# Kernel tuning notes

Hardware: AMD Instinct MI355X
Metric: run time of the kernel (lower is better)

Reference implementation:

```python
import jax, jax.numpy as jnp
import numpy as np

N = 50000
E = 1600000
D_IN, D_EMB, D_H, D_OUT, HEADS = 128, 128, 128, 64, 2


def setup_inputs() -> dict:
    key = jax.random.key(0)
    ks = jax.random.split(key, 12)
    return {
        "x": jax.random.normal(ks[0], (N, D_IN), jnp.float32),
        "edge_index": jax.random.randint(ks[1], (2, E), 0, N, dtype=jnp.int32),
        "node_indices": jnp.arange(N, dtype=jnp.int32),
        "emb": jax.random.normal(ks[2], (N, D_EMB), jnp.float32) * 0.1,
        "W_gcn": jax.random.normal(ks[3], (D_IN + D_EMB, D_H), jnp.float32) * 0.06,
        "b_gcn": jnp.zeros((D_H,), jnp.float32),
        "W_sage_l": jax.random.normal(ks[4], (D_H, D_H), jnp.float32) * 0.08,
        "W_sage_r": jax.random.normal(ks[5], (D_H, D_H), jnp.float32) * 0.08,
        "b_sage": jnp.zeros((D_H,), jnp.float32),
        "W_gat": jax.random.normal(ks[6], (D_H, HEADS, D_H), jnp.float32) * 0.08,
        "att_src": jax.random.normal(ks[7], (HEADS, D_H), jnp.float32) * 0.1,
        "att_dst": jax.random.normal(ks[8], (HEADS, D_H), jnp.float32) * 0.1,
        "b_gat": jnp.zeros((D_H,), jnp.float32),
        "W_out": jax.random.normal(ks[9], (D_H, D_OUT), jnp.float32) * 0.08,
        "b_out": jnp.zeros((D_OUT,), jnp.float32),
    }


def _forward(x, edge_index, node_indices, emb, W_gcn, b_gcn,
             W_sage_l, W_sage_r, b_sage, W_gat, att_src, att_dst, b_gat,
             W_out, b_out):
    n = x.shape[0]
    seg = jax.ops.segment_sum
    loops = jnp.arange(n, dtype=edge_index.dtype)

    # node2vec embedding lookup + concat
    h = jnp.concatenate([x, emb[node_indices]], axis=1)  # [N, D_IN+D_EMB]

    # --- GCNConv (symmetric norm, self loops) ---
    src = jnp.concatenate([edge_index[0], loops])
    dst = jnp.concatenate([edge_index[1], loops])
    deg = seg(jnp.ones_like(dst, jnp.float32), dst, num_segments=n)
    dinv = jnp.where(deg > 0, jax.lax.rsqrt(jnp.maximum(deg, 1.0)), 0.0)
    norm = dinv[src] * dinv[dst]                     # [E+N]
    hW = h @ W_gcn                                   # [N, D_H]
    h = seg(hW[src] * norm[:, None], dst, num_segments=n) + b_gcn
    h = jax.nn.relu(h)

    # --- SAGEConv (mean aggregation, no self loops) ---
    s, d = edge_index[0], edge_index[1]
    agg = seg(h[s], d, num_segments=n)
    cnt = seg(jnp.ones_like(d, jnp.float32), d, num_segments=n)
    mean = agg / jnp.maximum(cnt, 1.0)[:, None]
    h = mean @ W_sage_l + h @ W_sage_r + b_sage
    h = jax.nn.relu(h)

    # --- GATConv heads=2, concat=False (mean over heads), self loops ---
    xW = jnp.einsum('nd,dhc->nhc', h, W_gat)         # [N, H, D_H]
    a_src = jnp.einsum('nhc,hc->nh', xW, att_src)    # [N, H]
    a_dst = jnp.einsum('nhc,hc->nh', xW, att_dst)
    alpha = jax.nn.leaky_relu(a_src[src] + a_dst[dst], 0.2)  # [E+N, H]
    amax = jax.ops.segment_max(alpha, dst, num_segments=n)
    alpha = jnp.exp(alpha - amax[dst])
    asum = seg(alpha, dst, num_segments=n)
    alpha = alpha / (asum[dst] + 1e-16)
    out = seg(xW[src] * alpha[:, :, None], dst, num_segments=n)  # [N, H, D_H]
    h = jax.nn.relu(out.mean(axis=1) + b_gat)

    return h @ W_out + b_out


def reference(x, edge_index, node_indices, emb, W_gcn, b_gcn,
              W_sage_l, W_sage_r, b_sage, W_gat, att_src, att_dst, b_gat,
              W_out, b_out):
    return _forward(x, edge_index, node_indices, emb, W_gcn, b_gcn,
                    W_sage_l, W_sage_r, b_sage, W_gat, att_src, att_dst, b_gat,
                    W_out, b_out)
```

## Files before the change

### kernel.cpp

```cpp
#include <hip/hip_runtime.h>


typedef short bf16x8 __attribute__((ext_vector_type(8)));
typedef float f32x4  __attribute__((ext_vector_type(4)));

static __device__ __forceinline__ float leaky02(float x) {
    return x > 0.f ? x : 0.2f * x;
}
static __device__ __forceinline__ unsigned short f2bf(float f) {
    unsigned u = __float_as_uint(f);
    u = (u + 0x7FFFu + ((u >> 16) & 1u)) >> 16;
    return (unsigned short)u;
}
static __device__ __forceinline__ float bf2f(unsigned short h) {
    return __uint_as_float(((unsigned)h) << 16);
}
static __device__ __forceinline__ float4 bf4(ushort4 h) {
    return make_float4(bf2f(h.x), bf2f(h.y), bf2f(h.z), bf2f(h.w));
}
static __device__ __forceinline__ void split_bf(float v, unsigned short& h,
                                                unsigned short& l) {
    unsigned u = __float_as_uint(v);
    unsigned uh = u & 0xFFFF0000u;
    h = (unsigned short)(uh >> 16);
    l = f2bf(v - __uint_as_float(uh));
}

__global__ void deg_edges(const int* __restrict__ dst, int* __restrict__ degi, int E) {
    int e = blockIdx.x * blockDim.x + threadIdx.x;
    if (e < E) atomicAdd(&degi[dst[e]], 1);
}

__global__ __launch_bounds__(256)
void scan_part_norm(const int* __restrict__ degi, int* __restrict__ partial,
                    float* __restrict__ dinv, float* __restrict__ icnt, int n)
{
    int t = threadIdx.x;
    int base = blockIdx.x * 1024 + t * 4;
    int s = 0;
#pragma unroll
    for (int i = 0; i < 4; ++i) {
        int g = base + i;
        if (g < n) {
            int de = degi[g];
            s += de;
            dinv[g] = rsqrtf((float)(de + 1));
            icnt[g] = 1.0f / (float)(de > 1 ? de : 1);
        }
    }
#pragma unroll
    for (int m = 32; m > 0; m >>= 1) s += __shfl_xor(s, m, 64);
    __shared__ int wsum[4];
    if ((t & 63) == 0) wsum[t >> 6] = s;
    __syncthreads();
    if (t == 0) partial[blockIdx.x] = wsum[0] + wsum[1] + wsum[2] + wsum[3];
}

__global__ __launch_bounds__(64)
void scan_offsets(int* __restrict__ partial, int nb)
{
    int t = threadIdx.x;
    int carry = 0;
    for (int base = 0; base < nb; base += 64) {
        int i = base + t;
        int v = (i < nb) ? partial[i] : 0;
        int incl = v;
#pragma unroll
        for (int m = 1; m < 64; m <<= 1) {
            int o = __shfl_up(incl, m, 64);
            if (t >= m) incl += o;
        }
        if (i < nb) partial[i] = incl - v + carry;
        carry += __shfl(incl, 63, 64);
    }
}

__global__ __launch_bounds__(256)
void scan_write(const int* __restrict__ degi, const int* __restrict__ partial,
                int* __restrict__ rowptr, int n)
{
    __shared__ int tmp[256];
    int t = threadIdx.x;
    int base = blockIdx.x * 1024 + t * 4;
    int v[4]; int s = 0;
#pragma unroll
    for (int i = 0; i < 4; ++i) {
        int g = base + i;
        v[i] = (g < n) ? degi[g] : 0;
        s += v[i];
    }
    tmp[t] = s;
    __syncthreads();
    for (int off = 1; off < 256; off <<= 1) {
        int a = (t >= off) ? tmp[t - off] : 0;
        __syncthreads();
        tmp[t] += a;
        __syncthreads();
    }
    int run = tmp[t] - s + partial[blockIdx.x];
#pragma unroll
    for (int i = 0; i < 4; ++i) {
        int g = base + i;
        if (g < n) rowptr[g] = run;
        run += v[i];
    }
}

__global__ void csr_fill(const int* __restrict__ src, const int* __restrict__ dst,
                         int* __restrict__ rowptr, int* __restrict__ csr, int E)
{
    int e = blockIdx.x * blockDim.x + threadIdx.x;
    if (e >= E) return;
    int d = dst[e];
    int pos = atomicAdd(&rowptr[d], 1);
    csr[pos] = src[e];
}

template<bool HAS_A2, bool RELU, bool HAS_BIAS, bool HAS_IDX, bool SCALE,
         bool ATT, bool OUT_BF16, bool A_BF16>
__global__ __launch_bounds__(256)
void gemm_mfma(const void* __restrict__ A1, const float* __restrict__ W1,
               const void* __restrict__ A2, const float* __restrict__ W2,
               const int* __restrict__ idx2, const float* __restrict__ bias,
               const float* __restrict__ scale,
               const float* __restrict__ att_src, const float* __restrict__ att_dst,
               float* __restrict__ a_s, float* __restrict__ a_d,
               float* __restrict__ C, int nrows, int ncW, int ncC)
{
    __shared__ unsigned short ABh[8][65][8];
    __shared__ unsigned short WBh[8][65][8], WBl[8][65][8];
    const int t    = threadIdx.x;
    const int lane = t & 63;
    const int wv   = t >> 6;
    const int l15  = lane & 15;
    const int lg   = lane >> 4;
    const int row0 = blockIdx.x * 128;
    const int colOff = blockIdx.y * 128;

    f32x4 acc[2][8];
#pragma unroll
    for (int mt = 0; mt < 2; ++mt)
#pragma unroll
        for (int nt = 0; nt < 8; ++nt) acc[mt][nt] = (f32x4){0.f, 0.f, 0.f, 0.f};

    const int npass = HAS_A2 ? 2 : 1;
    for (int p = 0; p < npass; ++p) {
        const void* A = (p == 0) ? A1 : A2;
        const float* W = (p == 0) ? W1 : W2;
        for (int kt = 0; kt < 4; ++kt) {
            if (A_BF16) {
                const unsigned short* Ab = (const unsigned short*)A;
#pragma unroll
                for (int i = 0; i < 2; ++i) {
                    int f = i * 256 + t;
                    int r = f >> 2, kq = f & 3;
                    int row = row0 + r; if (row >= nrows) row = nrows - 1;
                    int arow = (p == 1 && HAS_IDX) ? idx2[row] : row;
                    bf16x8 v = *(const bf16x8*)(Ab + (size_t)arow * 128 + kt * 32 + kq * 8);
                    *(bf16x8*)&ABh[r >> 4][(r & 15) + (kq << 4)][0] = v;
                }
            } else {
                const float* Af = (const float*)A;
#pragma unroll
                for (int i = 0; i < 4; ++i) {
                    int f = i * 256 + t;
                    int r = f >> 3, c4 = (f & 7) << 2;
                    int row = row0 + r; if (row >= nrows) row = nrows - 1;
                    int arow = (p == 1 && HAS_IDX) ? idx2[row] : row;
                    float4 v = *(const float4*)(Af + (size_t)arow * 128 + kt * 32 + c4);
                    int slot = (r & 15) + ((c4 >> 3) << 4);
                    *(ushort4*)&ABh[r >> 4][slot][c4 & 4] =
                        make_ushort4(f2bf(v.x), f2bf(v.y), f2bf(v.z), f2bf(v.w));
                }
            }
#pragma unroll
            for (int i = 0; i < 4; ++i) {
                int f = i * 256 + t;
                int wr = f >> 5, wc4 = (f & 31) << 2;
                float4 v = *(const float4*)(W + (size_t)(kt * 32 + wr) * ncW + colOff + wc4);
                int jj = wr & 7, kg16 = (wr >> 3) << 4;
                int nt = wc4 >> 4, sb = (wc4 & 15) + kg16;
                unsigned short h, l;
                split_bf(v.x, h, l); WBh[nt][sb + 0][jj] = h; WBl[nt][sb + 0][jj] = l;
                split_bf(v.y, h, l); WBh[nt][sb + 1][jj] = h; WBl[nt][sb + 1][jj] = l;
                split_bf(v.z, h, l); WBh[nt][sb + 2][jj] = h; WBl[nt][sb + 2][jj] = l;
                split_bf(v.w, h, l); WBh[nt][sb + 3][jj] = h; WBl[nt][sb + 3][jj] = l;
            }
            __syncthreads();
            bf16x8 a0 = *reinterpret_cast<const bf16x8*>(&ABh[wv * 2 + 0][lane][0]);
            bf16x8 a1 = *reinterpret_cast<const bf16x8*>(&ABh[wv * 2 + 1][lane][0]);
#pragma unroll
            for (int nt = 0; nt < 8; ++nt) {
                bf16x8 bh = *reinterpret_cast<const bf16x8*>(&WBh[nt][lane][0]);
                bf16x8 bl = *reinterpret_cast<const bf16x8*>(&WBl[nt][lane][0]);
                acc[0][nt] = __builtin_amdgcn_mfma_f32_16x16x32_bf16(a0, bl, acc[0][nt], 0, 0, 0);
                acc[0][nt] = __builtin_amdgcn_mfma_f32_16x16x32_bf16(a0, bh, acc[0][nt], 0, 0, 0);
                acc[1][nt] = __builtin_amdgcn_mfma_f32_16x16x32_bf16(a1, bl, acc[1][nt], 0, 0, 0);
                acc[1][nt] = __builtin_amdgcn_mfma_f32_16x16x32_bf16(a1, bh, acc[1][nt], 0, 0, 0);
            }
            __syncthreads();
        }
    }

    float bias_v[8], as_v[8], ad_v[8];
#pragma unroll
    for (int nt = 0; nt < 8; ++nt) {
        int col = colOff + nt * 16 + l15;
        if (HAS_BIAS) bias_v[nt] = bias[col];
        if (ATT) { as_v[nt] = att_src[col]; ad_v[nt] = att_dst[col]; }
    }
#pragma unroll
    for (int mt = 0; mt < 2; ++mt) {
#pragma unroll
        for (int reg = 0; reg < 4; ++reg) {
            int row = row0 + wv * 32 + mt * 16 + lg * 4 + reg;
            bool ok = row < nrows;
            float sc = 1.f;
            if (SCALE) sc = ok ? scale[row] : 0.f;
            float vv[8];
            float ps = 0.f, pd = 0.f;
#pragma unroll
            for (int nt = 0; nt < 8; ++nt) {
                float v = acc[mt][nt][reg];
                if (SCALE) v *= sc;
                if (HAS_BIAS) v += bias_v[nt];
                if (RELU) v = fmaxf(v, 0.f);
                vv[nt] = v;
                if (ATT) { ps = fmaf(v, as_v[nt], ps); pd = fmaf(v, ad_v[nt], pd); }
            }
            if (ok) {
                if (OUT_BF16) {
                    unsigned short* cp =
                        (unsigned short*)C + (size_t)row * ncC + colOff + l15;
#pragma unroll
                    for (int nt = 0; nt < 8; ++nt) cp[nt * 16] = f2bf(vv[nt]);
                } else {
                    float* cp = C + (size_t)row * ncC + colOff + l15;
#pragma unroll
                    for (int nt = 0; nt < 8; ++nt) cp[nt * 16] = vv[nt];
                }
            }
            if (ATT) {
#pragma unroll
                for (int m = 1; m < 16; m <<= 1) {
                    ps += __shfl_xor(ps, m, 64);
                    pd += __shfl_xor(pd, m, 64);
                }
                if (ok && l15 == 0) {
                    a_s[row * 2 + blockIdx.y] = ps;
                    a_d[row * 2 + blockIdx.y] = pd;
                }
            }
        }
    }
}

__global__ __launch_bounds__(256)
void gcn_gather(const int* __restrict__ rowptr, const int* __restrict__ csr,
                const float* __restrict__ dinv,
                const unsigned short* __restrict__ hWb,
                const float* __restrict__ b,
                unsigned short* __restrict__ h1b, int n)
{
    int d = blockIdx.x * 4 + (threadIdx.x >> 6);
    if (d >= n) return;
    int lane = threadIdx.x & 63;
    int half = lane >> 5;
    int c = (lane & 31) << 2;
    int r1 = rowptr[d];
    int r0 = (d == 0) ? 0 : rowptr[d - 1];
    float4 acc = make_float4(0.f, 0.f, 0.f, 0.f);
    int j = r0 + half;
    for (; j + 6 < r1; j += 8) {
        int s0 = csr[j], s1 = csr[j + 2], s2 = csr[j + 4], s3 = csr[j + 6];
        float4 v0 = bf4(*(const ushort4*)(hWb + (size_t)s0 * 128 + c));
        float4 v1 = bf4(*(const ushort4*)(hWb + (size_t)s1 * 128 + c));
        float4 v2 = bf4(*(const ushort4*)(hWb + (size_t)s2 * 128 + c));
        float4 v3 = bf4(*(const ushort4*)(hWb + (size_t)s3 * 128 + c));
        acc.x += (v0.x + v1.x) + (v2.x + v3.x);
        acc.y += (v0.y + v1.y) + (v2.y + v3.y);
        acc.z += (v0.z + v1.z) + (v2.z + v3.z);
        acc.w += (v0.w + v1.w) + (v2.w + v3.w);
    }
    for (; j < r1; j += 2) {
        int s = csr[j];
        float4 v = bf4(*(const ushort4*)(hWb + (size_t)s * 128 + c));
        acc.x += v.x; acc.y += v.y; acc.z += v.z; acc.w += v.w;
    }
    acc.x += __shfl_xor(acc.x, 32, 64);
    acc.y += __shfl_xor(acc.y, 32, 64);
    acc.z += __shfl_xor(acc.z, 32, 64);
    acc.w += __shfl_xor(acc.w, 32, 64);
    if (lane < 32) {
        float dd = dinv[d];
        float4 vd = bf4(*(const ushort4*)(hWb + (size_t)d * 128 + c));
        float4 bb = *(const float4*)(b + c);
        float o0 = fmaxf(fmaf(acc.x + vd.x, dd, bb.x), 0.f);
        float o1 = fmaxf(fmaf(acc.y + vd.y, dd, bb.y), 0.f);
        float o2 = fmaxf(fmaf(acc.z + vd.z, dd, bb.z), 0.f);
        float o3 = fmaxf(fmaf(acc.w + vd.w, dd, bb.w), 0.f);
        *(ushort4*)(h1b + (size_t)d * 128 + c) =
            make_ushort4(f2bf(o0), f2bf(o1), f2bf(o2), f2bf(o3));
    }
}

__global__ __launch_bounds__(256)
void sage_gather(const int* __restrict__ rowptr, const int* __restrict__ csr,
                 const float* __restrict__ icnt,
                 const unsigned short* __restrict__ h1b,
                 unsigned short* __restrict__ meanb, int n)
{
    int d = blockIdx.x * 4 + (threadIdx.x >> 6);
    if (d >= n) return;
    int lane = threadIdx.x & 63;
    int half = lane >> 5;
    int c = (lane & 31) << 2;
    int r1 = rowptr[d];
    int r0 = (d == 0) ? 0 : rowptr[d - 1];
    float4 acc = make_float4(0.f, 0.f, 0.f, 0.f);
    int j = r0 + half;
    for (; j + 6 < r1; j += 8) {
        int s0 = csr[j], s1 = csr[j + 2], s2 = csr[j + 4], s3 = csr[j + 6];
        float4 v0 = bf4(*(const ushort4*)(h1b + (size_t)s0 * 128 + c));
        float4 v1 = bf4(*(const ushort4*)(h1b + (size_t)s1 * 128 + c));
        float4 v2 = bf4(*(const ushort4*)(h1b + (size_t)s2 * 128 + c));
        float4 v3 = bf4(*(const ushort4*)(h1b + (size_t)s3 * 128 + c));
        acc.x += (v0.x + v1.x) + (v2.x + v3.x);
        acc.y += (v0.y + v1.y) + (v2.y + v3.y);
        acc.z += (v0.z + v1.z) + (v2.z + v3.z);
        acc.w += (v0.w + v1.w) + (v2.w + v3.w);
    }
    for (; j < r1; j += 2) {
        int s = csr[j];
        float4 v = bf4(*(const ushort4*)(h1b + (size_t)s * 128 + c));
        acc.x += v.x; acc.y += v.y; acc.z += v.z; acc.w += v.w;
    }
    acc.x += __shfl_xor(acc.x, 32, 64);
    acc.y += __shfl_xor(acc.y, 32, 64);
    acc.z += __shfl_xor(acc.z, 32, 64);
    acc.w += __shfl_xor(acc.w, 32, 64);
    if (lane < 32) {
        float ic = icnt[d];
        *(ushort4*)(meanb + (size_t)d * 128 + c) =
            make_ushort4(f2bf(acc.x * ic), f2bf(acc.y * ic),
                         f2bf(acc.z * ic), f2bf(acc.w * ic));
    }
}

__global__ __launch_bounds__(256)
void gat_gather(const int* __restrict__ rowptr, const int* __restrict__ csr,
                const float* __restrict__ a_s, const float* __restrict__ a_d,
                const unsigned short* __restrict__ xWb,
                const float* __restrict__ b_gat,
                const float* __restrict__ W_out, const float* __restrict__ b_out,
                float* __restrict__ out, int n)
{
    __shared__ float h3row[4][128];
    int wv = threadIdx.x >> 6;
    int d = blockIdx.x * 4 + wv;
    if (d >= n) return;
    int lane = threadIdx.x & 63;
    const int hoff = lane >> 5;
    const int hsel = lane & 32;
    int r1 = rowptr[d];
    int r0 = (d == 0) ? 0 : rowptr[d - 1];
    const int nE = r1 - r0;
    const float adh = a_d[d * 2 + hoff];

    float4 acc = make_float4(0.f, 0.f, 0.f, 0.f);
    float wacc = 0.f;

    for (int blk = 0; blk < nE; blk += 32) {
        int eidx = blk + (lane & 31);
        int s_l = d;
        float wl = 0.f;
        if (eidx < nE) {
            s_l = csr[r0 + eidx];
            wl = __expf(leaky02(a_s[s_l * 2 + hoff] + adh));
        }
        wacc += wl;
        int cnt = min(32, nE - blk);
        int e = 0;
        for (; e + 4 <= cnt; e += 4) {
            int   s0 = __shfl(s_l, e + 0, 64), s1 = __shfl(s_l, e + 1, 64);
            int   s2 = __shfl(s_l, e + 2, 64), s3 = __shfl(s_l, e + 3, 64);
            float w0 = __shfl(wl, (e + 0) | hsel, 64);
            float w1 = __shfl(wl, (e + 1) | hsel, 64);
            float w2 = __shfl(wl, (e + 2) | hsel, 64);
            float w3 = __shfl(wl, (e + 3) | hsel, 64);
            float4 v0 = bf4(((const ushort4*)(xWb + (size_t)s0 * 256))[lane]);
            float4 v1 = bf4(((const ushort4*)(xWb + (size_t)s1 * 256))[lane]);
            float4 v2 = bf4(((const ushort4*)(xWb + (size_t)s2 * 256))[lane]);
            float4 v3 = bf4(((const ushort4*)(xWb + (size_t)s3 * 256))[lane]);
            acc.x = fmaf(v0.x, w0, fmaf(v1.x, w1, fmaf(v2.x, w2, fmaf(v3.x, w3, acc.x))));
            acc.y = fmaf(v0.y, w0, fmaf(v1.y, w1, fmaf(v2.y, w2, fmaf(v3.y, w3, acc.y))));
            acc.z = fmaf(v0.z, w0, fmaf(v1.z, w1, fmaf(v2.z, w2, fmaf(v3.z, w3, acc.z))));
            acc.w = fmaf(v0.w, w0, fmaf(v1.w, w1, fmaf(v2.w, w2, fmaf(v3.w, w3, acc.w))));
        }
        for (; e < cnt; ++e) {
            int   s = __shfl(s_l, e, 64);
            float w = __shfl(wl, e | hsel, 64);
            float4 v = bf4(((const ushort4*)(xWb + (size_t)s * 256))[lane]);
            acc.x = fmaf(v.x, w, acc.x);
            acc.y = fmaf(v.y, w, acc.y);
            acc.z = fmaf(v.z, w, acc.z);
            acc.w = fmaf(v.w, w, acc.w);
        }
    }

    float wself = __expf(leaky02(a_s[d * 2 + hoff] + adh));
    {
        float4 v = bf4(((const ushort4*)(xWb + (size_t)d * 256))[lane]);
        acc.x = fmaf(v.x, wself, acc.x);
        acc.y = fmaf(v.y, wself, acc.y);
        acc.z = fmaf(v.z, wself, acc.z);
        acc.w = fmaf(v.w, wself, acc.w);
    }
#pragma unroll
    for (int sh = 16; sh > 0; sh >>= 1) wacc += __shfl_xor(wacc, sh, 64);
    float inv = 1.f / (wacc + wself + 1e-16f);
    acc.x *= inv; acc.y *= inv; acc.z *= inv; acc.w *= inv;

    float c0 = acc.x + __shfl_xor(acc.x, 32, 64);
    float c1 = acc.y + __shfl_xor(acc.y, 32, 64);
    float c2 = acc.z + __shfl_xor(acc.z, 32, 64);
    float c3 = acc.w + __shfl_xor(acc.w, 32, 64);
    if (lane < 32) {
        float4 bb = ((const float4*)b_gat)[lane];
        float4 o;
        o.x = fmaxf(0.5f * c0 + bb.x, 0.f);
        o.y = fmaxf(0.5f * c1 + bb.y, 0.f);
        o.z = fmaxf(0.5f * c2 + bb.z, 0.f);
        o.w = fmaxf(0.5f * c3 + bb.w, 0.f);
        ((float4*)h3row[wv])[lane] = o;
    }
    __threadfence_block();
    const float* hr = h3row[wv];
    float t0 = 0.f, t1 = 0.f, t2 = 0.f, t3 = 0.f;
#pragma unroll 8
    for (int k = 0; k < 128; k += 4) {
        t0 = fmaf(hr[k + 0], W_out[(k + 0) * 64 + lane], t0);
        t1 = fmaf(hr[k + 1], W_out[(k + 1) * 64 + lane], t1);
        t2 = fmaf(hr[k + 2], W_out[(k + 2) * 64 + lane], t2);
        t3 = fmaf(hr[k + 3], W_out[(k + 3) * 64 + lane], t3);
    }
    out[(size_t)d * 64 + lane] = (t0 + t1) + (t2 + t3) + b_out[lane];
}

extern "C" void kernel_launch(void* const* d_in, const int* in_sizes, int n_in,
                              void* d_out, int out_size, void* d_ws, size_t ws_size,
                              hipStream_t stream)
{
    const float* x      = (const float*)d_in[0];
    const int*   ei     = (const int*)d_in[1];
    const int*   nidx   = (const int*)d_in[2];
    const float* emb    = (const float*)d_in[3];
    const float* W_gcn  = (const float*)d_in[4];
    const float* b_gcn  = (const float*)d_in[5];
    const float* W_sl   = (const float*)d_in[6];
    const float* W_sr   = (const float*)d_in[7];
    const float* b_sage = (const float*)d_in[8];
    const float* W_gat  = (const float*)d_in[9];
    const float* att_s  = (const float*)d_in[10];
    const float* att_d  = (const float*)d_in[11];
    const float* b_gat  = (const float*)d_in[12];
    const float* W_out  = (const float*)d_in[13];
    const float* b_out  = (const float*)d_in[14];
    float* out = (float*)d_out;

    const int n = in_sizes[0] / 128;
    const int E = in_sizes[1] / 2;
    const int* esrc = ei;
    const int* edst = ei + E;

    const size_t P = (size_t)n * 128;
    const int nb_scan = (n + 1023) / 1024;
    float* ws = (float*)d_ws;
    unsigned short* hWb   = (unsigned short*)ws;
    unsigned short* h1b   = (unsigned short*)(ws + P / 2);
    unsigned short* meanb = (unsigned short*)(ws + P);
    unsigned short* h2b   = (unsigned short*)(ws + 3 * P / 2);
    unsigned short* xWb   = (unsigned short*)(ws + 2 * P);
    float* dinv = ws + 3 * P;
    float* icnt = dinv + n;
    float* a_s  = icnt + n;
    float* a_d  = a_s + 2 * n;
    int* degi   = (int*)(a_d + 2 * n);
    int* rowptr = degi + n;
    int* partial= rowptr + n;
    int* csr    = partial + nb_scan + 1;

    const int TB = 256;
    int nblk_e     = (E + TB - 1) / TB;
    int nblk_wav_n = (n + 3) / 4;
    int gemm_rows  = (n + 127) / 128;

    hipMemsetAsync(degi, 0, (size_t)n * sizeof(int), stream);
    deg_edges<<<nblk_e, TB, 0, stream>>>(edst, degi, E);
    scan_part_norm<<<nb_scan, TB, 0, stream>>>(degi, partial, dinv, icnt, n);
    scan_offsets<<<1, 64, 0, stream>>>(partial, nb_scan);
    scan_write<<<nb_scan, TB, 0, stream>>>(degi, partial, rowptr, n);
    csr_fill<<<nblk_e, TB, 0, stream>>>(esrc, edst, rowptr, csr, E);

    gemm_mfma<true, false, false, true, true, false, true, false>
        <<<dim3(gemm_rows, 1), TB, 0, stream>>>(
        x, W_gcn, emb, W_gcn + 128 * 128, nidx, nullptr, dinv,
        nullptr, nullptr, nullptr, nullptr, (float*)hWb, n, 128, 128);
    gcn_gather<<<nblk_wav_n, TB, 0, stream>>>(rowptr, csr, dinv, hWb, b_gcn,
                                              h1b, n);

    sage_gather<<<nblk_wav_n, TB, 0, stream>>>(rowptr, csr, icnt, h1b, meanb, n);
    gemm_mfma<true, true, true, false, false, false, true, true>
        <<<dim3(gemm_rows, 1), TB, 0, stream>>>(
        meanb, W_sl, h1b, W_sr, nullptr, b_sage, nullptr,
        nullptr, nullptr, nullptr, nullptr, (float*)h2b, n, 128, 128);

    gemm_mfma<false, false, false, false, false, true, true, true>
        <<<dim3(gemm_rows, 2), TB, 0, stream>>>(
        h2b, W_gat, nullptr, nullptr, nullptr, nullptr, nullptr,
        att_s, att_d, a_s, a_d, (float*)xWb, n, 256, 256);
    gat_gather<<<nblk_wav_n, TB, 0, stream>>>(rowptr, csr, a_s, a_d, xWb, b_gat,
                                              W_out, b_out, out, n);
}
```

Baseline: 631.1 us.

## Fuse SAGE GEMM and GAT projection GEMM, keeping h2 tile in shared memory

Merges the SAGE linear layer and the GAT projection into one kernel. The ReLU'd bf16 h2 tile stays in LDS and feeds two 128-column chunks of the W_gat GEMM, so h2 no longer makes a round trip through global memory and one launch disappears. The GAT step now runs serially within each block instead of across a 2-wide grid. The extra ~34KB of LDS per block may reduce occupancy. The GCN GEMM is split into its own specialized kernel without template flags.

```diff
diff --git a/kernel.cpp b/kernel.cpp
--- a/kernel.cpp
+++ b/kernel.cpp
@@ -116,16 +116,30 @@
     csr[pos] = src[e];
 }
 
-template<bool HAS_A2, bool RELU, bool HAS_BIAS, bool HAS_IDX, bool SCALE,
-         bool ATT, bool OUT_BF16, bool A_BF16>
-__global__ __launch_bounds__(256)
-void gemm_mfma(const void* __restrict__ A1, const float* __restrict__ W1,
-               const void* __restrict__ A2, const float* __restrict__ W2,
-               const int* __restrict__ idx2, const float* __restrict__ bias,
-               const float* __restrict__ scale,
-               const float* __restrict__ att_src, const float* __restrict__ att_dst,
-               float* __restrict__ a_s, float* __restrict__ a_d,
-               float* __restrict__ C, int nrows, int ncW, int ncC)
+static __device__ __forceinline__ void stage_w_split(
+    const float* __restrict__ W, int ncW, int colOff, int kt, int t,
+    unsigned short (*WBh)[65][8], unsigned short (*WBl)[65][8])
+{
+#pragma unroll
+    for (int i = 0; i < 4; ++i) {
+        int f = i * 256 + t;
+        int wr = f >> 5, wc4 = (f & 31) << 2;
+        float4 v = *(const float4*)(W + (size_t)(kt * 32 + wr) * ncW + colOff + wc4);
+        int jj = wr & 7, kg16 = (wr >> 3) << 4;
+        int nt = wc4 >> 4, sb = (wc4 & 15) + kg16;
+        unsigned short h, l;
+        split_bf(v.x, h, l); WBh[nt][sb + 0][jj] = h; WBl[nt][sb + 0][jj] = l;
+        split_bf(v.y, h, l); WBh[nt][sb + 1][jj] = h; WBl[nt][sb + 1][jj] = l;
+        split_bf(v.z, h, l); WBh[nt][sb + 2][jj] = h; WBl[nt][sb + 2][jj] = l;
+        split_bf(v.w, h, l); WBh[nt][sb + 3][jj] = h; WBl[nt][sb + 3][jj] = l;
+    }
+}
+
+__global__ __launch_bounds__(256)
+void gemm_gcn(const float* __restrict__ A1, const float* __restrict__ W1,
+              const float* __restrict__ A2, const float* __restrict__ W2,
+              const int* __restrict__ idx2, const float* __restrict__ scale,
+              unsigned short* __restrict__ C, int nrows)
 {
     __shared__ unsigned short ABh[8][65][8];
     __shared__ unsigned short WBh[8][65][8], WBl[8][65][8];
@@ -135,7 +149,6 @@
     const int l15  = lane & 15;
     const int lg   = lane >> 4;
     const int row0 = blockIdx.x * 128;
-    const int colOff = blockIdx.y * 128;
 
     f32x4 acc[2][8];
 #pragma unroll
@@ -143,49 +156,22 @@
 #pragma unroll
         for (int nt = 0; nt < 8; ++nt) acc[mt][nt] = (f32x4){0.f, 0.f, 0.f, 0.f};
 
-    const int npass = HAS_A2 ? 2 : 1;
-    for (int p = 0; p < npass; ++p) {
-        const void* A = (p == 0) ? A1 : A2;
+    for (int p = 0; p < 2; ++p) {
+        const float* A = (p == 0) ? A1 : A2;
         const float* W = (p == 0) ? W1 : W2;
         for (int kt = 0; kt < 4; ++kt) {
-            if (A_BF16) {
-                const unsigned short* Ab = (const unsigned short*)A;
-#pragma unroll
-                for (int i = 0; i < 2; ++i) {
-                    int f = i * 256 + t;
-                    int r = f >> 2, kq = f & 3;
-                    int row = row0 + r; if (row >= nrows) row = nrows - 1;
-                    int arow = (p == 1 && HAS_IDX) ? idx2[row] : row;
-                    bf16x8 v = *(const bf16x8*)(Ab + (size_t)arow * 128 + kt * 32 + kq * 8);
-                    *(bf16x8*)&ABh[r >> 4][(r & 15) + (kq << 4)][0] = v;
-                }
-            } else {
-                const float* Af = (const float*)A;
-#pragma unroll
-                for (int i = 0; i < 4; ++i) {
-                    int f = i * 256 + t;
-                    int r = f >> 3, c4 = (f & 7) << 2;
-                    int row = row0 + r; if (row >= nrows) row = nrows - 1;
-                    int arow = (p == 1 && HAS_IDX) ? idx2[row] : row;
-                    float4 v = *(const float4*)(Af + (size_t)arow * 128 + kt * 32 + c4);
-                    int slot = (r & 15) + ((c4 >> 3) << 4);
-                    *(ushort4*)&ABh[r >> 4][slot][c4 & 4] =
-                        make_ushort4(f2bf(v.x), f2bf(v.y), f2bf(v.z), f2bf(v.w));
-                }
-            }
 #pragma unroll
             for (int i = 0; i < 4; ++i) {
                 int f = i * 256 + t;
-                int wr = f >> 5, wc4 = (f & 31) << 2;
-                float4 v = *(const float4*)(W + (size_t)(kt * 32 + wr) * ncW + colOff + wc4);
-                int jj = wr & 7, kg16 = (wr >> 3) << 4;
-                int nt = wc4 >> 4, sb = (wc4 & 15) + kg16;
-                unsigned short h, l;
-                split_bf(v.x, h, l); WBh[nt][sb + 0][jj] = h; WBl[nt][sb + 0][jj] = l;
-                split_bf(v.y, h, l); WBh[nt][sb + 1][jj] = h; WBl[nt][sb + 1][jj] = l;
-                split_bf(v.z, h, l); WBh[nt][sb + 2][jj] = h; WBl[nt][sb + 2][jj] = l;
-                split_bf(v.w, h, l); WBh[nt][sb + 3][jj] = h; WBl[nt][sb + 3][jj] = l;
-            }
+                int r = f >> 3, c4 = (f & 7) << 2;
+                int row = row0 + r; if (row >= nrows) row = nrows - 1;
+                int arow = (p == 1) ? idx2[row] : row;
+                float4 v = *(const float4*)(A + (size_t)arow * 128 + kt * 32 + c4);
+                int slot = (r & 15) + ((c4 >> 3) << 4);
+                *(ushort4*)&ABh[r >> 4][slot][c4 & 4] =
+                    make_ushort4(f2bf(v.x), f2bf(v.y), f2bf(v.z), f2bf(v.w));
+            }
+            stage_w_split(W, 128, 0, kt, t, WBh, WBl);
             __syncthreads();
             bf16x8 a0 = *reinterpret_cast<const bf16x8*>(&ABh[wv * 2 + 0][lane][0]);
             bf16x8 a1 = *reinterpret_cast<const bf16x8*>(&ABh[wv * 2 + 1][lane][0]);
@@ -201,54 +187,149 @@
             __syncthreads();
         }
     }
-
-    float bias_v[8], as_v[8], ad_v[8];
-#pragma unroll
-    for (int nt = 0; nt < 8; ++nt) {
-        int col = colOff + nt * 16 + l15;
-        if (HAS_BIAS) bias_v[nt] = bias[col];
-        if (ATT) { as_v[nt] = att_src[col]; ad_v[nt] = att_dst[col]; }
-    }
 #pragma unroll
     for (int mt = 0; mt < 2; ++mt) {
 #pragma unroll
         for (int reg = 0; reg < 4; ++reg) {
             int row = row0 + wv * 32 + mt * 16 + lg * 4 + reg;
-            bool ok = row < nrows;
-            float sc = 1.f;
-            if (SCALE) sc = ok ? scale[row] : 0.f;
-            float vv[8];
-            float ps = 0.f, pd = 0.f;
+            if (row >= nrows) continue;
+            float sc = scale[row];
+            unsigned short* cp = C + (size_t)row * 128 + l15;
+#pragma unroll
+            for (int nt = 0; nt < 8; ++nt)
+                cp[nt * 16] = f2bf(acc[mt][nt][reg] * sc);
+        }
+    }
+}
+
+__global__ __launch_bounds__(256)
+void gemm_sage_gat(const unsigned short* __restrict__ meanb,
+                   const float* __restrict__ W_sl,
+                   const unsigned short* __restrict__ h1b,
+                   const float* __restrict__ W_sr,
+                   const float* __restrict__ b_sage,
+                   const float* __restrict__ W_gat,
+                   const float* __restrict__ att_src,
+                   const float* __restrict__ att_dst,
+                   float* __restrict__ a_s, float* __restrict__ a_d,
+                   unsigned short* __restrict__ xWb, int nrows)
+{
+    __shared__ unsigned short ABh[8][65][8];
+    __shared__ unsigned short WBh[8][65][8], WBl[8][65][8];
+    __shared__ unsigned short H2[128][136];
+    const int t    = threadIdx.x;
+    const int lane = t & 63;
+    const int wv   = t >> 6;
+    const int l15  = lane & 15;
+    const int lg   = lane >> 4;
+    const int row0 = blockIdx.x * 128;
+
+    f32x4 acc[2][8];
+#pragma unroll
+    for (int mt = 0; mt < 2; ++mt)
+#pragma unroll
+        for (int nt = 0; nt < 8; ++nt) acc[mt][nt] = (f32x4){0.f, 0.f, 0.f, 0.f};
+
+    for (int p = 0; p < 2; ++p) {
+        const unsigned short* A = (p == 0) ? meanb : h1b;
+        const float* W = (p == 0) ? W_sl : W_sr;
+        for (int kt = 0; kt < 4; ++kt) {
+#pragma unroll
+            for (int i = 0; i < 2; ++i) {
+                int f = i * 256 + t;
+                int r = f >> 2, kq = f & 3;
+                int row = row0 + r; if (row >= nrows) row = nrows - 1;
+                bf16x8 v = *(const bf16x8*)(A + (size_t)row * 128 + kt * 32 + kq * 8);
+                *(bf16x8*)&ABh[r >> 4][(r & 15) + (kq << 4)][0] = v;
+            }
+            stage_w_split(W, 128, 0, kt, t, WBh, WBl);
+            __syncthreads();
+            bf16x8 a0 = *reinterpret_cast<const bf16x8*>(&ABh[wv * 2 + 0][lane][0]);
+            bf16x8 a1 = *reinterpret_cast<const bf16x8*>(&ABh[wv * 2 + 1][lane][0]);
 #pragma unroll
             for (int nt = 0; nt < 8; ++nt) {
-                float v = acc[mt][nt][reg];
-                if (SCALE) v *= sc;
-                if (HAS_BIAS) v += bias_v[nt];
-                if (RELU) v = fmaxf(v, 0.f);
-                vv[nt] = v;
-                if (ATT) { ps = fmaf(v, as_v[nt], ps); pd = fmaf(v, ad_v[nt], pd); }
-            }
-            if (ok) {
-                if (OUT_BF16) {
-                    unsigned short* cp =
-                        (unsigned short*)C + (size_t)row * ncC + colOff + l15;
-#pragma unroll
-                    for (int nt = 0; nt < 8; ++nt) cp[nt * 16] = f2bf(vv[nt]);
-                } else {
-                    float* cp = C + (size_t)row * ncC + colOff + l15;
-#pragma unroll
-                    for (int nt = 0; nt < 8; ++nt) cp[nt * 16] = vv[nt];
+                bf16x8 bh = *reinterpret_cast<const bf16x8*>(&WBh[nt][lane][0]);
+                bf16x8 bl = *reinterpret_cast<const bf16x8*>(&WBl[nt][lane][0]);
+                acc[0][nt] = __builtin_amdgcn_mfma_f32_16x16x32_bf16(a0, bl, acc[0][nt], 0, 0, 0);
+                acc[0][nt] = __builtin_amdgcn_mfma_f32_16x16x32_bf16(a0, bh, acc[0][nt], 0, 0, 0);
+                acc[1][nt] = __builtin_amdgcn_mfma_f32_16x16x32_bf16(a1, bl, acc[1][nt], 0, 0, 0);
+                acc[1][nt] = __builtin_amdgcn_mfma_f32_16x16x32_bf16(a1, bh, acc[1][nt], 0, 0, 0);
+            }
+            __syncthreads();
+        }
+    }
+    {
+        float bias_v[8];
+#pragma unroll
+        for (int nt = 0; nt < 8; ++nt) bias_v[nt] = b_sage[nt * 16 + l15];
+#pragma unroll
+        for (int mt = 0; mt < 2; ++mt) {
+#pragma unroll
+            for (int reg = 0; reg < 4; ++reg) {
+                int r = wv * 32 + mt * 16 + lg * 4 + reg;
+#pragma unroll
+                for (int nt = 0; nt < 8; ++nt) {
+                    float v = fmaxf(acc[mt][nt][reg] + bias_v[nt], 0.f);
+                    H2[r][nt * 16 + l15] = f2bf(v);
                 }
             }
-            if (ATT) {
+        }
+    }
+    __syncthreads();
+
+    for (int ch = 0; ch < 2; ++ch) {
+        f32x4 acc2[2][8];
+#pragma unroll
+        for (int mt = 0; mt < 2; ++mt)
+#pragma unroll
+            for (int nt = 0; nt < 8; ++nt) acc2[mt][nt] = (f32x4){0.f, 0.f, 0.f, 0.f};
+        for (int kt = 0; kt < 4; ++kt) {
+            stage_w_split(W_gat, 256, ch * 128, kt, t, WBh, WBl);
+            __syncthreads();
+            bf16x8 a0 = *(const bf16x8*)&H2[(wv * 2 + 0) * 16 + l15][kt * 32 + lg * 8];
+            bf16x8 a1 = *(const bf16x8*)&H2[(wv * 2 + 1) * 16 + l15][kt * 32 + lg * 8];
+#pragma unroll
+            for (int nt = 0; nt < 8; ++nt) {
+                bf16x8 bh = *reinterpret_cast<const bf16x8*>(&WBh[nt][lane][0]);
+                bf16x8 bl = *reinterpret_cast<const bf16x8*>(&WBl[nt][lane][0]);
+                acc2[0][nt] = __builtin_amdgcn_mfma_f32_16x16x32_bf16(a0, bl, acc2[0][nt], 0, 0, 0);
+                acc2[0][nt] = __builtin_amdgcn_mfma_f32_16x16x32_bf16(a0, bh, acc2[0][nt], 0, 0, 0);
+                acc2[1][nt] = __builtin_amdgcn_mfma_f32_16x16x32_bf16(a1, bl, acc2[1][nt], 0, 0, 0);
+                acc2[1][nt] = __builtin_amdgcn_mfma_f32_16x16x32_bf16(a1, bh, acc2[1][nt], 0, 0, 0);
+            }
+            __syncthreads();
+        }
+        float as_v[8], ad_v[8];
+#pragma unroll
+        for (int nt = 0; nt < 8; ++nt) {
+            int col = ch * 128 + nt * 16 + l15;
+            as_v[nt] = att_src[col];
+            ad_v[nt] = att_dst[col];
+        }
+#pragma unroll
+        for (int mt = 0; mt < 2; ++mt) {
+#pragma unroll
+            for (int reg = 0; reg < 4; ++reg) {
+                int row = row0 + wv * 32 + mt * 16 + lg * 4 + reg;
+                bool ok = row < nrows;
+                float ps = 0.f, pd = 0.f;
+                unsigned short* cp =
+                    xWb + (size_t)row * 256 + ch * 128 + l15;
+#pragma unroll
+                for (int nt = 0; nt < 8; ++nt) {
+                    float v = acc2[mt][nt][reg];
+                    if (ok) cp[nt * 16] = f2bf(v);
+                    ps = fmaf(v, as_v[nt], ps);
+                    pd = fmaf(v, ad_v[nt], pd);
+                }
 #pragma unroll
                 for (int m = 1; m < 16; m <<= 1) {
                     ps += __shfl_xor(ps, m, 64);
                     pd += __shfl_xor(pd, m, 64);
                 }
                 if (ok && l15 == 0) {
-                    a_s[row * 2 + blockIdx.y] = ps;
-                    a_d[row * 2 + blockIdx.y] = pd;
+                    a_s[row * 2 + ch] = ps;
+                    a_d[row * 2 + ch] = pd;
                 }
             }
         }
@@ -479,9 +560,8 @@
     unsigned short* hWb   = (unsigned short*)ws;
     unsigned short* h1b   = (unsigned short*)(ws + P / 2);
     unsigned short* meanb = (unsigned short*)(ws + P);
-    unsigned short* h2b   = (unsigned short*)(ws + 3 * P / 2);
-    unsigned short* xWb   = (unsigned short*)(ws + 2 * P);
-    float* dinv = ws + 3 * P;
+    unsigned short* xWb   = (unsigned short*)(ws + 3 * P / 2);
+    float* dinv = ws + 5 * P / 2;
     float* icnt = dinv + n;
     float* a_s  = icnt + n;
     float* a_d  = a_s + 2 * n;
@@ -502,23 +582,15 @@
     scan_write<<<nb_scan, TB, 0, stream>>>(degi, partial, rowptr, n);
     csr_fill<<<nblk_e, TB, 0, stream>>>(esrc, edst, rowptr, csr, E);
 
-    gemm_mfma<true, false, false, true, true, false, true, false>
-        <<<dim3(gemm_rows, 1), TB, 0, stream>>>(
-        x, W_gcn, emb, W_gcn + 128 * 128, nidx, nullptr, dinv,
-        nullptr, nullptr, nullptr, nullptr, (float*)hWb, n, 128, 128);
+    gemm_gcn<<<gemm_rows, TB, 0, stream>>>(
+        x, W_gcn, emb, W_gcn + 128 * 128, nidx, dinv, hWb, n);
     gcn_gather<<<nblk_wav_n, TB, 0, stream>>>(rowptr, csr, dinv, hWb, b_gcn,
                                               h1b, n);
 
     sage_gather<<<nblk_wav_n, TB, 0, stream>>>(rowptr, csr, icnt, h1b, meanb, n);
-    gemm_mfma<true, true, true, false, false, false, true, true>
-        <<<dim3(gemm_rows, 1), TB, 0, stream>>>(
-        meanb, W_sl, h1b, W_sr, nullptr, b_sage, nullptr,
-        nullptr, nullptr, nullptr, nullptr, (float*)h2b, n, 128, 128);
-
-    gemm_mfma<false, false, false, false, false, true, true, true>
-        <<<dim3(gemm_rows, 2), TB, 0, stream>>>(
-        h2b, W_gat, nullptr, nullptr, nullptr, nullptr, nullptr,
-        att_s, att_d, a_s, a_d, (float*)xWb, n, 256, 256);
+    gemm_sage_gat<<<gemm_rows, TB, 0, stream>>>(
+        meanb, W_sl, h1b, W_sr, b_sage, W_gat, att_s, att_d, a_s, a_d, xWb, n);
+
     gat_gather<<<nblk_wav_n, TB, 0, stream>>>(rowptr, csr, a_s, a_d, xWb, b_gat,
                                               W_out, b_out, out, n);
 }
```

Measured after the change: 612.9 us. -2.9%, faster.
